# Optimization experiments

Measured on AMD Instinct MI355X. Metric: run time of the kernel, lower is better.

## Reference

```python
import jax, jax.numpy as jnp
import numpy as np

N_NODES = 50000
N_EDGES = 800000
IN_CH, HID_CH, OUT_CH = 128, 128, 64


def setup_inputs() -> dict:
    key = jax.random.key(0)
    k1, k2, k3, k4, k5, k6 = jax.random.split(key, 6)
    x = jax.random.normal(k1, (N_NODES, IN_CH), dtype=jnp.float32)
    edge_index = jax.random.randint(k2, (2, N_EDGES), 0, N_NODES, dtype=jnp.int64)
    # nn.Linear params: W [out, in], b [out]
    W1 = jax.random.normal(k3, (HID_CH, IN_CH), dtype=jnp.float32) / np.sqrt(IN_CH)
    b1 = jax.random.normal(k4, (HID_CH,), dtype=jnp.float32) * 0.01
    W2 = jax.random.normal(k5, (OUT_CH, HID_CH), dtype=jnp.float32) / np.sqrt(HID_CH)
    b2 = jax.random.normal(k6, (OUT_CH,), dtype=jnp.float32) * 0.01
    return {"x": x, "edge_index": edge_index, "W1": W1, "b1": b1, "W2": W2, "b2": b2}


def _aggregate(x, edge_index):
    # Faithful to SimpleGNN.aggregate: deg from ROW counts, normalization gathered at DST (col).
    row, col = edge_index[0], edge_index[1]
    n = x.shape[0]
    deg = jnp.bincount(row, length=n).astype(x.dtype)
    deg_inv = jnp.where(deg > 0, 1.0 / deg, 0.0)
    # out[dst] += x[src] * deg_inv[dst]  ==  segment_sum(x[src] by dst) * deg_inv[dst]
    agg = jax.ops.segment_sum(x[row], col, num_segments=n)
    return agg * deg_inv[:, None]


def reference(x, edge_index, W1, b1, W2, b2):
    h = x @ W1.T + b1                 # [N, hidden]
    h = _aggregate(h, edge_index)     # degree-normalized scatter-add
    out = h @ W2.T + b2               # [N, out]
    return out
```

## Files before the change

kernel.cpp:

```cpp
#include <hip/hip_runtime.h>
#include <hip/hip_bf16.h>


#define IN_CH   128
#define OUT_CH  64
#define NCHUNK  64
#define LGCHUNK 6
#define NRANGE  8
#define RBINS   6272
#define MC_BLOCKS 33

typedef unsigned short u16;
typedef unsigned int u32;

static __device__ inline float bfu32_lo(u32 u) {
    u32 v = u << 16; return __uint_as_float(v);
}
static __device__ inline float bfu32_hi(u32 u) {
    u32 v = u & 0xffff0000u; return __uint_as_float(v);
}
static __device__ inline u16 f2bf(float f) {
    __hip_bfloat16 h = __float2bfloat16(f);
    return *reinterpret_cast<u16*>(&h);
}

static __device__ inline int detect_stride(const int* ei) {
    int f = 1;
    for (int i = 1; i < 64; i += 2)
        if (ei[i] != 0) { f = 0; break; }
    return 1 + f;
}

__global__ __launch_bounds__(256) void mk_prep(const float* __restrict__ W1,
                                               const float* __restrict__ b1,
                                               const float* __restrict__ W2,
                                               const int* __restrict__ ei,
                                               float* __restrict__ M,
                                               float* __restrict__ c,
                                               u16* __restrict__ row_slab,
                                               u16* __restrict__ col_slab,
                                               int n_edges, int n_nodes) {
    __shared__ u32 bins[RBINS];
    __shared__ int s_stride;
    int b = blockIdx.x;
    if (b < MC_BLOCKS) {
        int tid = b * 256 + threadIdx.x;
        if (tid < IN_CH * OUT_CH) {
            int o = tid & (OUT_CH - 1);
            int i = tid >> 6;
            float acc = 0.f;
            for (int h = 0; h < 128; ++h)
                acc += W1[h * 128 + i] * W2[o * 128 + h];
            M[i * OUT_CH + o] = acc;
        } else if (tid < IN_CH * OUT_CH + OUT_CH) {
            int o = tid - IN_CH * OUT_CH;
            float acc = 0.f;
            for (int h = 0; h < 128; ++h)
                acc += b1[h] * W2[o * 128 + h];
            c[o] = acc;
        }
        return;
    }
    int hb = b - MC_BLOCKS;
    int chunk = hb & (NCHUNK - 1);
    int range = hb >> LGCHUNK;

    int range_size = (n_nodes + NRANGE - 1) / NRANGE;
    int lo = range * range_size;
    int hi = lo + range_size; if (hi > n_nodes) hi = n_nodes;
    int nbins = hi - lo;
    if (nbins <= 0) return;

    if (threadIdx.x == 0) s_stride = detect_stride(ei);
    for (int i = threadIdx.x; i < nbins; i += 256) bins[i] = 0u;
    __syncthreads();
    int stride = s_stride;

    size_t e0 = (size_t)chunk * n_edges / NCHUNK;
    size_t e1 = (size_t)(chunk + 1) * n_edges / NCHUNK;
    size_t cnt = e1 - e0;
    const int* rp = ei;
    const int* cp = ei + (size_t)n_edges * stride;

    size_t i = threadIdx.x;
    for (; i + 768 < cnt; i += 1024) {
        int s0 = rp[(e0 + i) * stride];
        int s1 = rp[(e0 + i + 256) * stride];
        int s2 = rp[(e0 + i + 512) * stride];
        int s3 = rp[(e0 + i + 768) * stride];
        int d0 = cp[(e0 + i) * stride];
        int d1 = cp[(e0 + i + 256) * stride];
        int d2 = cp[(e0 + i + 512) * stride];
        int d3 = cp[(e0 + i + 768) * stride];
        if (s0 >= lo && s0 < hi) atomicAdd(&bins[s0 - lo], 1u);
        if (s1 >= lo && s1 < hi) atomicAdd(&bins[s1 - lo], 1u);
        if (s2 >= lo && s2 < hi) atomicAdd(&bins[s2 - lo], 1u);
        if (s3 >= lo && s3 < hi) atomicAdd(&bins[s3 - lo], 1u);
        if (d0 >= lo && d0 < hi && (unsigned)s0 < (unsigned)n_nodes) atomicAdd(&bins[d0 - lo], 0x10000u);
        if (d1 >= lo && d1 < hi && (unsigned)s1 < (unsigned)n_nodes) atomicAdd(&bins[d1 - lo], 0x10000u);
        if (d2 >= lo && d2 < hi && (unsigned)s2 < (unsigned)n_nodes) atomicAdd(&bins[d2 - lo], 0x10000u);
        if (d3 >= lo && d3 < hi && (unsigned)s3 < (unsigned)n_nodes) atomicAdd(&bins[d3 - lo], 0x10000u);
    }
    for (; i < cnt; i += 256) {
        int s = rp[(e0 + i) * stride];
        int d = cp[(e0 + i) * stride];
        if (s >= lo && s < hi) atomicAdd(&bins[s - lo], 1u);
        if (d >= lo && d < hi && (unsigned)s < (unsigned)n_nodes) atomicAdd(&bins[d - lo], 0x10000u);
    }
    __syncthreads();

    size_t base = (size_t)chunk * n_nodes + lo;
    for (int k = threadIdx.x; k < nbins; k += 256) {
        u32 v = bins[k];
        row_slab[base + k] = (u16)(v & 0xFFFFu);
        col_slab[base + k] = (u16)(v >> 16);
    }
}

__global__ __launch_bounds__(256) void mk_y_choff(const float* __restrict__ x,
                                                  const float* __restrict__ M,
                                                  u16* __restrict__ y,
                                                  u16* __restrict__ row_slab,
                                                  u16* __restrict__ col_slab,
                                                  int* __restrict__ deg_row,
                                                  int* __restrict__ cnt_col,
                                                  int* __restrict__ cursor_part,
                                                  int* __restrict__ bsums,
                                                  int n_nodes, int y_blocks) {
    __shared__ float smem[IN_CH * OUT_CH + 64 * (IN_CH + 4)];
    int b = blockIdx.x;
    int tid = threadIdx.x;

    if (b < y_blocks) {
        float* Ms = smem;
        float (*xs)[IN_CH + 4] = (float(*)[IN_CH + 4])(smem + IN_CH * OUT_CH);
        int tx = tid & 15;
        int ty = tid >> 4;
        int row0 = b * 64;

        const float4* Mv = (const float4*)M;
        float4* Msv = (float4*)Ms;
#pragma unroll
        for (int k = 0; k < 8; ++k) Msv[tid + 256 * k] = Mv[tid + 256 * k];

        for (int f = tid; f < 64 * 32; f += 256) {
            int r = f >> 5, kq = f & 31;
            float4 v = make_float4(0.f, 0.f, 0.f, 0.f);
            if (row0 + r < n_nodes)
                v = *(const float4*)&x[(size_t)(row0 + r) * IN_CH + 4 * kq];
            *(float4*)&xs[r][4 * kq] = v;
        }
        __syncthreads();

        float4 acc[4];
#pragma unroll
        for (int j = 0; j < 4; ++j) acc[j] = make_float4(0.f, 0.f, 0.f, 0.f);

        for (int k = 0; k < IN_CH; k += 4) {
            float4 xr[4], mr[4];
#pragma unroll
            for (int j = 0; j < 4; ++j)
                xr[j] = *(const float4*)&xs[4 * ty + j][k];
#pragma unroll
            for (int kk = 0; kk < 4; ++kk)
                mr[kk] = *(const float4*)&Ms[(k + kk) * OUT_CH + 4 * tx];
#pragma unroll
            for (int j = 0; j < 4; ++j) {
                acc[j].x = fmaf(xr[j].x, mr[0].x, acc[j].x);
                acc[j].y = fmaf(xr[j].x, mr[0].y, acc[j].y);
                acc[j].z = fmaf(xr[j].x, mr[0].z, acc[j].z);
                acc[j].w = fmaf(xr[j].x, mr[0].w, acc[j].w);
                acc[j].x = fmaf(xr[j].y, mr[1].x, acc[j].x);
                acc[j].y = fmaf(xr[j].y, mr[1].y, acc[j].y);
                acc[j].z = fmaf(xr[j].y, mr[1].z, acc[j].z);
                acc[j].w = fmaf(xr[j].y, mr[1].w, acc[j].w);
                acc[j].x = fmaf(xr[j].z, mr[2].x, acc[j].x);
                acc[j].y = fmaf(xr[j].z, mr[2].y, acc[j].y);
                acc[j].z = fmaf(xr[j].z, mr[2].z, acc[j].z);
                acc[j].w = fmaf(xr[j].z, mr[2].w, acc[j].w);
                acc[j].x = fmaf(xr[j].w, mr[3].x, acc[j].x);
                acc[j].y = fmaf(xr[j].w, mr[3].y, acc[j].y);
                acc[j].z = fmaf(xr[j].w, mr[3].z, acc[j].z);
                acc[j].w = fmaf(xr[j].w, mr[3].w, acc[j].w);
            }
        }

#pragma unroll
        for (int j = 0; j < 4; ++j) {
            int r = row0 + 4 * ty + j;
            if (r < n_nodes) {
                ushort4 s4;
                s4.x = f2bf(acc[j].x);
                s4.y = f2bf(acc[j].y);
                s4.z = f2bf(acc[j].z);
                s4.w = f2bf(acc[j].w);
                *(ushort4*)&y[(size_t)r * OUT_CH + 4 * tx] = s4;
            }
        }
        return;
    }

    int* sm = (int*)smem;
    int t = tid;
    int n = (b - y_blocks) * 256 + t;
    int run = 0;
    if (n < n_nodes) {
        int sum = 0;
#pragma unroll 8
        for (int ch = 0; ch < NCHUNK; ++ch)
            sum += row_slab[(size_t)ch * n_nodes + n];
        deg_row[n] = sum;
#pragma unroll 8
        for (int ch = 0; ch < NCHUNK; ++ch) {
            int v = col_slab[(size_t)ch * n_nodes + n];
            col_slab[(size_t)ch * n_nodes + n] = (u16)run;
            run += v;
        }
        cnt_col[n] = run;
    }
    sm[t] = run;
    __syncthreads();
    for (int d = 1; d < 256; d <<= 1) {
        int add = (t >= d) ? sm[t - d] : 0;
        __syncthreads();
        sm[t] += add;
        __syncthreads();
    }
    if (n < n_nodes) cursor_part[n] = sm[t] - run;
    if (t == 255) bsums[b - y_blocks] = sm[t];
}

static __device__ inline void block_bscan(const int* __restrict__ bsums, int nb,
                                          int* __restrict__ bscan) {
    int t = threadIdx.x;
    int v = (t < nb) ? bsums[t] : 0;
    bscan[t] = v;
    __syncthreads();
    for (int d = 1; d < 256; d <<= 1) {
        int add = (t >= d) ? bscan[t - d] : 0;
        __syncthreads();
        bscan[t] += add;
        __syncthreads();
    }
    bscan[t] -= v;
    __syncthreads();
}

__global__ __launch_bounds__(256) void mk_place(const int* __restrict__ ei,
                                                const int* __restrict__ cursor_part,
                                                const int* __restrict__ bsums,
                                                const u16* __restrict__ col_slab,
                                                int* __restrict__ csr_src,
                                                int n_edges, int n_nodes, int nb) {
    __shared__ int rank[RBINS];
    __shared__ int bscan[256];
    block_bscan(bsums, nb, bscan);

    int b = blockIdx.x;
    int chunk = b & (NCHUNK - 1);
    int range = b >> LGCHUNK;

    int range_size = (n_nodes + NRANGE - 1) / NRANGE;
    int lo = range * range_size;
    int hi = lo + range_size; if (hi > n_nodes) hi = n_nodes;
    if (hi <= lo) return;

    for (int i = threadIdx.x; i < hi - lo; i += 256) rank[i] = 0;
    __syncthreads();

    int stride = detect_stride(ei);
    size_t e0 = (size_t)chunk * n_edges / NCHUNK;
    size_t e1 = (size_t)(chunk + 1) * n_edges / NCHUNK;
    size_t cnt = e1 - e0;
    const int* rp = ei;
    const int* cp = ei + (size_t)n_edges * stride;
    size_t slab_base = (size_t)chunk * n_nodes;

    size_t i = threadIdx.x;
    for (; i + 768 < cnt; i += 1024) {
        int s0 = rp[(e0 + i) * stride];
        int s1 = rp[(e0 + i + 256) * stride];
        int s2 = rp[(e0 + i + 512) * stride];
        int s3 = rp[(e0 + i + 768) * stride];
        int d0 = cp[(e0 + i) * stride];
        int d1 = cp[(e0 + i + 256) * stride];
        int d2 = cp[(e0 + i + 512) * stride];
        int d3 = cp[(e0 + i + 768) * stride];
        if (d0 >= lo && d0 < hi && (unsigned)s0 < (unsigned)n_nodes) {
            int r = atomicAdd(&rank[d0 - lo], 1);
            csr_src[cursor_part[d0] + bscan[d0 >> 8] + (int)col_slab[slab_base + d0] + r] = s0;
        }
        if (d1 >= lo && d1 < hi && (unsigned)s1 < (unsigned)n_nodes) {
            int r = atomicAdd(&rank[d1 - lo], 1);
            csr_src[cursor_part[d1] + bscan[d1 >> 8] + (int)col_slab[slab_base + d1] + r] = s1;
        }
        if (d2 >= lo && d2 < hi && (unsigned)s2 < (unsigned)n_nodes) {
            int r = atomicAdd(&rank[d2 - lo], 1);
            csr_src[cursor_part[d2] + bscan[d2 >> 8] + (int)col_slab[slab_base + d2] + r] = s2;
        }
        if (d3 >= lo && d3 < hi && (unsigned)s3 < (unsigned)n_nodes) {
            int r = atomicAdd(&rank[d3 - lo], 1);
            csr_src[cursor_part[d3] + bscan[d3 >> 8] + (int)col_slab[slab_base + d3] + r] = s3;
        }
    }
    for (; i < cnt; i += 256) {
        int s = rp[(e0 + i) * stride];
        int d = cp[(e0 + i) * stride];
        if (d >= lo && d < hi && (unsigned)s < (unsigned)n_nodes) {
            int r = atomicAdd(&rank[d - lo], 1);
            csr_src[cursor_part[d] + bscan[d >> 8] + (int)col_slab[slab_base + d] + r] = s;
        }
    }
}

__global__ __launch_bounds__(256) void mk_agg_final(const int* __restrict__ cursor_part,
                                                    const int* __restrict__ bsums,
                                                    const int* __restrict__ cnt_col,
                                                    const int* __restrict__ csr_src,
                                                    const int* __restrict__ deg_row,
                                                    const u32* __restrict__ y,
                                                    const float* __restrict__ c,
                                                    const float* __restrict__ b2,
                                                    float* __restrict__ out,
                                                    int n_nodes, int nb) {
    __shared__ int bscan[256];
    block_bscan(bsums, nb, bscan);

    int wave = threadIdx.x >> 6;
    int half = (threadIdx.x >> 5) & 1;
    int sub  = threadIdx.x & 31;
    int d = blockIdx.x * 8 + wave * 2 + half;
    if (d >= n_nodes) return;

    int start = cursor_part[d] + bscan[d >> 8];
    int cnt = cnt_col[d];
    int end = start + cnt;
    float ax = 0.f, ay = 0.f;
    int e1m = end - 1;
    for (int j = start; j < end; j += 8) {
        int i1 = j + 1 > e1m ? e1m : j + 1;
        int i2 = j + 2 > e1m ? e1m : j + 2;
        int i3 = j + 3 > e1m ? e1m : j + 3;
        int i4 = j + 4 > e1m ? e1m : j + 4;
        int i5 = j + 5 > e1m ? e1m : j + 5;
        int i6 = j + 6 > e1m ? e1m : j + 6;
        int i7 = j + 7 > e1m ? e1m : j + 7;
        int s0 = csr_src[j];
        int s1 = csr_src[i1];
        int s2 = csr_src[i2];
        int s3 = csr_src[i3];
        int s4 = csr_src[i4];
        int s5 = csr_src[i5];
        int s6 = csr_src[i6];
        int s7 = csr_src[i7];
        u32 u0 = y[(size_t)s0 * 32 + sub];
        u32 u1 = y[(size_t)s1 * 32 + sub];
        u32 u2 = y[(size_t)s2 * 32 + sub];
        u32 u3 = y[(size_t)s3 * 32 + sub];
        u32 u4 = y[(size_t)s4 * 32 + sub];
        u32 u5 = y[(size_t)s5 * 32 + sub];
        u32 u6 = y[(size_t)s6 * 32 + sub];
        u32 u7 = y[(size_t)s7 * 32 + sub];
        u1 = (j + 1 < end) ? u1 : 0u;
        u2 = (j + 2 < end) ? u2 : 0u;
        u3 = (j + 3 < end) ? u3 : 0u;
        u4 = (j + 4 < end) ? u4 : 0u;
        u5 = (j + 5 < end) ? u5 : 0u;
        u6 = (j + 6 < end) ? u6 : 0u;
        u7 = (j + 7 < end) ? u7 : 0u;
        ax += ((bfu32_lo(u0) + bfu32_lo(u1)) + (bfu32_lo(u2) + bfu32_lo(u3)))
            + ((bfu32_lo(u4) + bfu32_lo(u5)) + (bfu32_lo(u6) + bfu32_lo(u7)));
        ay += ((bfu32_hi(u0) + bfu32_hi(u1)) + (bfu32_hi(u2) + bfu32_hi(u3)))
            + ((bfu32_hi(u4) + bfu32_hi(u5)) + (bfu32_hi(u6) + bfu32_hi(u7)));
    }
    int dr = deg_row[d];
    float di = (dr > 0) ? (1.0f / (float)dr) : 0.f;
    float2 cv = *(const float2*)&c[2 * sub];
    float2 bv = *(const float2*)&b2[2 * sub];
    float2 o;
    o.x = di * ax + di * (float)cnt * cv.x + bv.x;
    o.y = di * ay + di * (float)cnt * cv.y + bv.y;
    *(float2*)&out[(size_t)d * OUT_CH + 2 * sub] = o;
}

extern "C" void kernel_launch(void* const* d_in, const int* in_sizes, int n_in,
                              void* d_out, int out_size, void* d_ws, size_t ws_size,
                              hipStream_t stream) {
    const float* x  = (const float*)d_in[0];
    const int*   ei = (const int*)d_in[1];
    const float* W1 = (const float*)d_in[2];
    const float* b1 = (const float*)d_in[3];
    const float* W2 = (const float*)d_in[4];
    const float* b2 = (const float*)d_in[5];
    float* out = (float*)d_out;

    const int n_nodes = in_sizes[0] / IN_CH;
    const int n_edges = in_sizes[1] / 2;

    const size_t slab_bytes = (((size_t)NCHUNK * n_nodes * 2) + 127) & ~(size_t)127;
    const size_t csr_bytes  = ((size_t)n_edges * 4 + 127) & ~(size_t)127;

    char* ws = (char*)d_ws;
    float* M        = (float*)(ws);
    float* c        = (float*)(ws + 32768);
    int*   deg_row  = (int*)  (ws + 33152);
    int*   cnt_col  = (int*)  (ws + 233216);
    int*   cursor   = (int*)  (ws + 433280);
    int*   bsums    = (int*)  (ws + 633344);
    u16*   row_slab = (u16*)  (ws + 637440);
    u16*   col_slab = (u16*)  (ws + 637440 + slab_bytes);
    int*   csr_src  = (int*)  (ws + 637440 + 2 * slab_bytes);
    u16*   y        = (u16*)  (ws + 637440 + 2 * slab_bytes + csr_bytes);

    const int y_blocks = (n_nodes + 63) / 64;
    const int nb = (n_nodes + 255) / 256;

    mk_prep<<<MC_BLOCKS + NCHUNK * NRANGE, 256, 0, stream>>>(
        W1, b1, W2, ei, M, c, row_slab, col_slab, n_edges, n_nodes);

    mk_y_choff<<<y_blocks + nb, 256, 0, stream>>>(
        x, M, y, row_slab, col_slab, deg_row, cnt_col, cursor, bsums,
        n_nodes, y_blocks);

    mk_place<<<NCHUNK * NRANGE, 256, 0, stream>>>(
        ei, cursor, bsums, col_slab, csr_src, n_edges, n_nodes, nb);

    mk_agg_final<<<(n_nodes + 7) / 8, 256, 0, stream>>>(
        cursor, bsums, cnt_col, csr_src, deg_row, (const u32*)y, c, b2, out,
        n_nodes, nb);
}
```

Measured before the change: 162.1 us.

## Widen gather loads, retune chunk/range split, deepen edge-loop unrolling

The aggregation kernel now gives each destination node 16 lanes that load 8-byte bf16 quads (uint2) and write float4 outputs, so each block covers 16 nodes instead of 8. The histogram and placement kernels now switch from 64 edge chunks × 8 node ranges to 128 × 4, with larger shared bins. Their edge loops unroll 8-way, and the placement kernel hoists the cursor and slab loads ahead of the atomics to raise memory-level parallelism. The cost is more registers and larger shared-memory bins per block, which may lower occupancy. The slab workspace also doubles with NCHUNK, which could overflow the workspace if it was sized tightly.

```diff
diff --git a/kernel.cpp b/kernel.cpp
--- a/kernel.cpp
+++ b/kernel.cpp
@@ -4,10 +4,10 @@
 
 #define IN_CH   128
 #define OUT_CH  64
-#define NCHUNK  64
-#define LGCHUNK 6
-#define NRANGE  8
-#define RBINS   6272
+#define NCHUNK  128
+#define LGCHUNK 7
+#define NRANGE  4
+#define RBINS   12544
 #define MC_BLOCKS 33
 
 typedef unsigned short u16;
@@ -83,29 +83,25 @@
     const int* cp = ei + (size_t)n_edges * stride;
 
     size_t i = threadIdx.x;
-    for (; i + 768 < cnt; i += 1024) {
-        int s0 = rp[(e0 + i) * stride];
-        int s1 = rp[(e0 + i + 256) * stride];
-        int s2 = rp[(e0 + i + 512) * stride];
-        int s3 = rp[(e0 + i + 768) * stride];
-        int d0 = cp[(e0 + i) * stride];
-        int d1 = cp[(e0 + i + 256) * stride];
-        int d2 = cp[(e0 + i + 512) * stride];
-        int d3 = cp[(e0 + i + 768) * stride];
-        if (s0 >= lo && s0 < hi) atomicAdd(&bins[s0 - lo], 1u);
-        if (s1 >= lo && s1 < hi) atomicAdd(&bins[s1 - lo], 1u);
-        if (s2 >= lo && s2 < hi) atomicAdd(&bins[s2 - lo], 1u);
-        if (s3 >= lo && s3 < hi) atomicAdd(&bins[s3 - lo], 1u);
-        if (d0 >= lo && d0 < hi && (unsigned)s0 < (unsigned)n_nodes) atomicAdd(&bins[d0 - lo], 0x10000u);
-        if (d1 >= lo && d1 < hi && (unsigned)s1 < (unsigned)n_nodes) atomicAdd(&bins[d1 - lo], 0x10000u);
-        if (d2 >= lo && d2 < hi && (unsigned)s2 < (unsigned)n_nodes) atomicAdd(&bins[d2 - lo], 0x10000u);
-        if (d3 >= lo && d3 < hi && (unsigned)s3 < (unsigned)n_nodes) atomicAdd(&bins[d3 - lo], 0x10000u);
+    int s[8], d[8];
+    for (; i + 1792 < cnt; i += 2048) {
+#pragma unroll
+        for (int k = 0; k < 8; ++k) s[k] = rp[(e0 + i + 256 * k) * stride];
+#pragma unroll
+        for (int k = 0; k < 8; ++k) d[k] = cp[(e0 + i + 256 * k) * stride];
+#pragma unroll
+        for (int k = 0; k < 8; ++k) {
+            if (s[k] >= lo && s[k] < hi) atomicAdd(&bins[s[k] - lo], 1u);
+            if (d[k] >= lo && d[k] < hi && (unsigned)s[k] < (unsigned)n_nodes)
+                atomicAdd(&bins[d[k] - lo], 0x10000u);
+        }
     }
     for (; i < cnt; i += 256) {
-        int s = rp[(e0 + i) * stride];
-        int d = cp[(e0 + i) * stride];
-        if (s >= lo && s < hi) atomicAdd(&bins[s - lo], 1u);
-        if (d >= lo && d < hi && (unsigned)s < (unsigned)n_nodes) atomicAdd(&bins[d - lo], 0x10000u);
+        int ss = rp[(e0 + i) * stride];
+        int dd = cp[(e0 + i) * stride];
+        if (ss >= lo && ss < hi) atomicAdd(&bins[ss - lo], 1u);
+        if (dd >= lo && dd < hi && (unsigned)ss < (unsigned)n_nodes)
+            atomicAdd(&bins[dd - lo], 0x10000u);
     }
     __syncthreads();
 
@@ -277,38 +273,32 @@
     size_t slab_base = (size_t)chunk * n_nodes;
 
     size_t i = threadIdx.x;
-    for (; i + 768 < cnt; i += 1024) {
-        int s0 = rp[(e0 + i) * stride];
-        int s1 = rp[(e0 + i + 256) * stride];
-        int s2 = rp[(e0 + i + 512) * stride];
-        int s3 = rp[(e0 + i + 768) * stride];
-        int d0 = cp[(e0 + i) * stride];
-        int d1 = cp[(e0 + i + 256) * stride];
-        int d2 = cp[(e0 + i + 512) * stride];
-        int d3 = cp[(e0 + i + 768) * stride];
-        if (d0 >= lo && d0 < hi && (unsigned)s0 < (unsigned)n_nodes) {
-            int r = atomicAdd(&rank[d0 - lo], 1);
-            csr_src[cursor_part[d0] + bscan[d0 >> 8] + (int)col_slab[slab_base + d0] + r] = s0;
-        }
-        if (d1 >= lo && d1 < hi && (unsigned)s1 < (unsigned)n_nodes) {
-            int r = atomicAdd(&rank[d1 - lo], 1);
-            csr_src[cursor_part[d1] + bscan[d1 >> 8] + (int)col_slab[slab_base + d1] + r] = s1;
-        }
-        if (d2 >= lo && d2 < hi && (unsigned)s2 < (unsigned)n_nodes) {
-            int r = atomicAdd(&rank[d2 - lo], 1);
-            csr_src[cursor_part[d2] + bscan[d2 >> 8] + (int)col_slab[slab_base + d2] + r] = s2;
-        }
-        if (d3 >= lo && d3 < hi && (unsigned)s3 < (unsigned)n_nodes) {
-            int r = atomicAdd(&rank[d3 - lo], 1);
-            csr_src[cursor_part[d3] + bscan[d3 >> 8] + (int)col_slab[slab_base + d3] + r] = s3;
+    int s[8], d[8], cpart[8], coff[8];
+    for (; i + 1792 < cnt; i += 2048) {
+#pragma unroll
+        for (int k = 0; k < 8; ++k) s[k] = rp[(e0 + i + 256 * k) * stride];
+#pragma unroll
+        for (int k = 0; k < 8; ++k) d[k] = cp[(e0 + i + 256 * k) * stride];
+#pragma unroll
+        for (int k = 0; k < 8; ++k) {
+            int dc = (d[k] >= lo && d[k] < hi) ? d[k] : lo;
+            cpart[k] = cursor_part[dc];
+            coff[k]  = (int)col_slab[slab_base + dc];
+        }
+#pragma unroll
+        for (int k = 0; k < 8; ++k) {
+            if (d[k] >= lo && d[k] < hi && (unsigned)s[k] < (unsigned)n_nodes) {
+                int r = atomicAdd(&rank[d[k] - lo], 1);
+                csr_src[cpart[k] + bscan[d[k] >> 8] + coff[k] + r] = s[k];
+            }
         }
     }
     for (; i < cnt; i += 256) {
-        int s = rp[(e0 + i) * stride];
-        int d = cp[(e0 + i) * stride];
-        if (d >= lo && d < hi && (unsigned)s < (unsigned)n_nodes) {
-            int r = atomicAdd(&rank[d - lo], 1);
-            csr_src[cursor_part[d] + bscan[d >> 8] + (int)col_slab[slab_base + d] + r] = s;
+        int ss = rp[(e0 + i) * stride];
+        int dd = cp[(e0 + i) * stride];
+        if (dd >= lo && dd < hi && (unsigned)ss < (unsigned)n_nodes) {
+            int r = atomicAdd(&rank[dd - lo], 1);
+            csr_src[cursor_part[dd] + bscan[dd >> 8] + (int)col_slab[slab_base + dd] + r] = ss;
         }
     }
 }
@@ -318,7 +308,7 @@
                                                     const int* __restrict__ cnt_col,
                                                     const int* __restrict__ csr_src,
                                                     const int* __restrict__ deg_row,
-                                                    const u32* __restrict__ y,
+                                                    const uint2* __restrict__ yv,
                                                     const float* __restrict__ c,
                                                     const float* __restrict__ b2,
                                                     float* __restrict__ out,
@@ -327,60 +317,51 @@
     block_bscan(bsums, nb, bscan);
 
     int wave = threadIdx.x >> 6;
-    int half = (threadIdx.x >> 5) & 1;
-    int sub  = threadIdx.x & 31;
-    int d = blockIdx.x * 8 + wave * 2 + half;
+    int lane = threadIdx.x & 63;
+    int dsub = lane >> 4;
+    int ch   = lane & 15;
+    int d = blockIdx.x * 16 + wave * 4 + dsub;
     if (d >= n_nodes) return;
 
     int start = cursor_part[d] + bscan[d >> 8];
     int cnt = cnt_col[d];
     int end = start + cnt;
-    float ax = 0.f, ay = 0.f;
     int e1m = end - 1;
+    float a0 = 0.f, a1 = 0.f, a2 = 0.f, a3 = 0.f;
     for (int j = start; j < end; j += 8) {
-        int i1 = j + 1 > e1m ? e1m : j + 1;
-        int i2 = j + 2 > e1m ? e1m : j + 2;
-        int i3 = j + 3 > e1m ? e1m : j + 3;
-        int i4 = j + 4 > e1m ? e1m : j + 4;
-        int i5 = j + 5 > e1m ? e1m : j + 5;
-        int i6 = j + 6 > e1m ? e1m : j + 6;
-        int i7 = j + 7 > e1m ? e1m : j + 7;
-        int s0 = csr_src[j];
-        int s1 = csr_src[i1];
-        int s2 = csr_src[i2];
-        int s3 = csr_src[i3];
-        int s4 = csr_src[i4];
-        int s5 = csr_src[i5];
-        int s6 = csr_src[i6];
-        int s7 = csr_src[i7];
-        u32 u0 = y[(size_t)s0 * 32 + sub];
-        u32 u1 = y[(size_t)s1 * 32 + sub];
-        u32 u2 = y[(size_t)s2 * 32 + sub];
-        u32 u3 = y[(size_t)s3 * 32 + sub];
-        u32 u4 = y[(size_t)s4 * 32 + sub];
-        u32 u5 = y[(size_t)s5 * 32 + sub];
-        u32 u6 = y[(size_t)s6 * 32 + sub];
-        u32 u7 = y[(size_t)s7 * 32 + sub];
-        u1 = (j + 1 < end) ? u1 : 0u;
-        u2 = (j + 2 < end) ? u2 : 0u;
-        u3 = (j + 3 < end) ? u3 : 0u;
-        u4 = (j + 4 < end) ? u4 : 0u;
-        u5 = (j + 5 < end) ? u5 : 0u;
-        u6 = (j + 6 < end) ? u6 : 0u;
-        u7 = (j + 7 < end) ? u7 : 0u;
-        ax += ((bfu32_lo(u0) + bfu32_lo(u1)) + (bfu32_lo(u2) + bfu32_lo(u3)))
-            + ((bfu32_lo(u4) + bfu32_lo(u5)) + (bfu32_lo(u6) + bfu32_lo(u7)));
-        ay += ((bfu32_hi(u0) + bfu32_hi(u1)) + (bfu32_hi(u2) + bfu32_hi(u3)))
-            + ((bfu32_hi(u4) + bfu32_hi(u5)) + (bfu32_hi(u6) + bfu32_hi(u7)));
+        int idx[8], srcs[8];
+#pragma unroll
+        for (int k = 0; k < 8; ++k) {
+            int t = j + k;
+            idx[k] = t > e1m ? e1m : t;
+        }
+#pragma unroll
+        for (int k = 0; k < 8; ++k) srcs[k] = csr_src[idx[k]];
+        uint2 u[8];
+#pragma unroll
+        for (int k = 0; k < 8; ++k) u[k] = yv[(size_t)srcs[k] * 16 + ch];
+#pragma unroll
+        for (int k = 1; k < 8; ++k)
+            if (j + k >= end) { u[k].x = 0u; u[k].y = 0u; }
+#pragma unroll
+        for (int k = 0; k < 8; ++k) {
+            a0 += bfu32_lo(u[k].x);
+            a1 += bfu32_hi(u[k].x);
+            a2 += bfu32_lo(u[k].y);
+            a3 += bfu32_hi(u[k].y);
+        }
     }
     int dr = deg_row[d];
     float di = (dr > 0) ? (1.0f / (float)dr) : 0.f;
-    float2 cv = *(const float2*)&c[2 * sub];
-    float2 bv = *(const float2*)&b2[2 * sub];
-    float2 o;
-    o.x = di * ax + di * (float)cnt * cv.x + bv.x;
-    o.y = di * ay + di * (float)cnt * cv.y + bv.y;
-    *(float2*)&out[(size_t)d * OUT_CH + 2 * sub] = o;
+    float fc = di * (float)cnt;
+    float4 cv = ((const float4*)c)[ch];
+    float4 bv = ((const float4*)b2)[ch];
+    float4 o;
+    o.x = di * a0 + fc * cv.x + bv.x;
+    o.y = di * a1 + fc * cv.y + bv.y;
+    o.z = di * a2 + fc * cv.z + bv.z;
+    o.w = di * a3 + fc * cv.w + bv.w;
+    ((float4*)(out + (size_t)d * OUT_CH))[ch] = o;
 }
 
 extern "C" void kernel_launch(void* const* d_in, const int* in_sizes, int n_in,
@@ -425,7 +406,7 @@
     mk_place<<<NCHUNK * NRANGE, 256, 0, stream>>>(
         ei, cursor, bsums, col_slab, csr_src, n_edges, n_nodes, nb);
 
-    mk_agg_final<<<(n_nodes + 7) / 8, 256, 0, stream>>>(
-        cursor, bsums, cnt_col, csr_src, deg_row, (const u32*)y, c, b2, out,
+    mk_agg_final<<<(n_nodes + 15) / 16, 256, 0, stream>>>(
+        cursor, bsums, cnt_col, csr_src, deg_row, (const uint2*)y, c, b2, out,
         n_nodes, nb);
 }
```

Measured after the change: 163.7 us. About the same (+1.0%).
